# Performance work log

Measured on AMD Instinct MI355X. Metric: run time of the kernel, lower is better.

The kernel has to match this reference:

```python
import jax, jax.numpy as jnp
import numpy as np

B, L, D, H = 4, 2048, 512, 512


def setup_inputs() -> dict:
    key = jax.random.key(0)
    ks = jax.random.split(key, 7)
    scale = D ** (-0.5)
    return {
        "x": jax.random.normal(ks[0], (B, L, D), jnp.float32),
        "hidden": jax.random.normal(ks[1], (B, D, H), jnp.float32),
        "log_base_lr": jnp.asarray(np.log(0.01), jnp.float32),
        "log_base_weight_decay": jnp.asarray(np.log(0.99), jnp.float32),
        "Wq": jax.random.normal(ks[2], (H, D), jnp.float32) * scale,
        "Wk": jax.random.normal(ks[3], (H, D), jnp.float32) * scale,
        "Wv": jax.random.normal(ks[4], (D, D), jnp.float32) * scale,
        "fc_lr_w": jax.random.normal(ks[5], (1, D), jnp.float32) * scale,
        "fc_lr_b": jnp.zeros((1,), jnp.float32),
        "fc_wd_w": jax.random.normal(ks[6], (1, D), jnp.float32) * scale,
        "fc_wd_b": jnp.zeros((1,), jnp.float32),
    }


def reference(x, hidden, log_base_lr, log_base_weight_decay, Wq, Wk, Wv,
              fc_lr_w, fc_lr_b, fc_wd_w, fc_wd_b):
    b, l, d = x.shape
    W_prev = hidden                                      # (b, d, h)
    query = jnp.einsum('bld,hd->blh', x, Wq)             # (b, l, h)
    key = jnp.einsum('bld,hd->blh', x, Wk)               # (b, l, h)
    value = jnp.einsum('bld,ed->ble', x, Wv)             # (b, l, d)

    lr = jnp.exp(log_base_lr) * jax.nn.sigmoid(
        jnp.einsum('bld,d->bl', x, fc_lr_w[0]) + fc_lr_b[0])        # (b, l)
    log_weight_decay = jnp.log(
        jnp.exp(log_base_weight_decay) * jax.nn.sigmoid(
            jnp.einsum('bld,d->bl', x, fc_wd_w[0]) + fc_wd_b[0]))   # (b, l)

    # cross-chunk decay: exp of prefix-sum of log decays
    wd_cross = jnp.exp(jnp.cumsum(log_weight_decay, axis=1))        # (b, l)

    # inner-chunk decay mask: (b, m, l), strictly-upper cumsum then upper triu
    rep = jnp.broadcast_to(log_weight_decay[:, None, :], (b, l, l))
    wd_inner = jnp.triu(jnp.exp(jnp.cumsum(jnp.triu(rep, 1), axis=2)))

    kq = jnp.einsum('blh,bmh->blm', key, query)          # (b, l, m)
    mask_kq = kq * wd_inner                              # (b, l, m)

    WpK_V = jnp.einsum('bdh,blh->bld', W_prev, key) - value         # (b, l, d)

    y_inner = -jnp.einsum('bld,bl,blm->bld', WpK_V, lr, mask_kq)
    y_cross = jnp.einsum('bdh,blh,bl->bld', W_prev, key, wd_cross)
    y = y_inner + y_cross

    W_next_inner = -jnp.einsum('bld,bl,blh->bdh', WpK_V, lr * wd_inner[:, :, -1], key)
    W_next_cross = W_prev * wd_cross[:, -1][:, None, None]
    W_next = W_next_inner + W_next_cross
    return (y, W_next)
```

## Files before the change

### kernel.cpp

```cpp
#include <hip/hip_runtime.h>
#include <cstdint>
#include <cstddef>

#define B_ 4
#define L_ 2048
#define D_ 512
#define H_ 512
#define CH 64
#define NC (L_ / CH)
#define NS 4

typedef unsigned short u16;
typedef __attribute__((ext_vector_type(8))) short short8v;
typedef __attribute__((ext_vector_type(4))) float f32x4;

typedef __attribute__((address_space(3))) unsigned lds_uint;
typedef const __attribute__((address_space(1))) unsigned glob_uint;

__device__ __forceinline__ void glds16(const u16* g, const u16* l) {
    __builtin_amdgcn_global_load_lds((glob_uint*)g, (lds_uint*)l, 16, 0, 0);
}

__device__ __forceinline__ u16 bf16_rne(float x) {
    union { float f; unsigned u; } v; v.f = x;
    unsigned r = v.u + 0x7fffu + ((v.u >> 16) & 1u);
    return (u16)(r >> 16);
}
__device__ __forceinline__ float bf16_tof(u16 h) {
    union { unsigned u; float f; } v; v.u = ((unsigned)h) << 16;
    return v.f;
}

__global__ __launch_bounds__(256) void k_prep(
    const float* __restrict__ x, const float* __restrict__ flr_w, const float* __restrict__ flr_b,
    const float* __restrict__ fwd_w, const float* __restrict__ fwd_b,
    const float* __restrict__ lblr, const float* __restrict__ lbwd,
    float* __restrict__ lr, float* __restrict__ lwd, float* __restrict__ wd,
    u16* __restrict__ xh)
{
    int bx = blockIdx.x;
    int wave = threadIdx.x >> 6;
    int lane = threadIdx.x & 63;
    int row  = bx * 4 + wave;
    const float4* xr = (const float4*)(x + (size_t)row * D_);
    const float4* wl = (const float4*)flr_w;
    const float4* ww = (const float4*)fwd_w;
    float zl = 0.f, zw = 0.f;
#pragma unroll
    for (int i = 0; i < 2; ++i) {
        int idx = lane + i * 64;
        float4 xv = xr[idx];
        float4 av = wl[idx];
        float4 bv = ww[idx];
        zl += xv.x*av.x + xv.y*av.y + xv.z*av.z + xv.w*av.w;
        zw += xv.x*bv.x + xv.y*bv.y + xv.z*bv.z + xv.w*bv.w;
        ushort4 h4;
        h4.x = bf16_rne(xv.x); h4.y = bf16_rne(xv.y);
        h4.z = bf16_rne(xv.z); h4.w = bf16_rne(xv.w);
        *(ushort4*)(xh + (size_t)row * D_ + idx * 4) = h4;
    }
#pragma unroll
    for (int off = 32; off; off >>= 1) {
        zl += __shfl_xor(zl, off, 64);
        zw += __shfl_xor(zw, off, 64);
    }
    if (lane == 0) {
        zl += flr_b[0];
        zw += fwd_b[0];
        float lrv = expf(lblr[0]) / (1.f + expf(-zl));
        float ls = (zw >= 0.f) ? (-log1pf(expf(-zw))) : (zw - log1pf(expf(zw)));
        float lw = lbwd[0] + ls;
        lr[row]  = lrv;
        lwd[row] = lw;
        wd[row]  = expf(lw);
    }
}

__global__ __launch_bounds__(256) void k_cumsum(
    const float* __restrict__ lwd, const float* __restrict__ lr,
    const float* __restrict__ Wq, const float* __restrict__ Wk, const float* __restrict__ Wv,
    const float* __restrict__ hid,
    u16* __restrict__ Wqh, u16* __restrict__ Wkh, u16* __restrict__ Wvh, u16* __restrict__ Wph,
    float* __restrict__ cum, float* __restrict__ wdc, float* __restrict__ c)
{
    int bx = blockIdx.x;
    if (bx >= B_) {
        int idx = bx - B_;
        int y = idx >> 8;
        const size_t DH = (size_t)D_ * H_;
        const float* s; u16* d;
        if      (y == 0) { s = Wq; d = Wqh; }
        else if (y == 1) { s = Wk; d = Wkh; }
        else if (y == 2) { s = Wv; d = Wvh; }
        else             { s = hid + (size_t)(y - 3) * DH; d = Wph + (size_t)(y - 3) * DH; }
        int i = ((idx & 255) * 256 + threadIdx.x) * 4;
        float4 v = *(const float4*)(s + i);
        ushort4 h4;
        h4.x = bf16_rne(v.x); h4.y = bf16_rne(v.y);
        h4.z = bf16_rne(v.z); h4.w = bf16_rne(v.w);
        *(ushort4*)(d + i) = h4;
        return;
    }
    int b = bx;
    int t = threadIdx.x;
    const float* in = lwd + (size_t)b * L_;
    float v[8];
    float s = 0.f;
#pragma unroll
    for (int j = 0; j < 8; ++j) { s += in[t*8 + j]; v[j] = s; }
    __shared__ float sd[256];
    __shared__ float totb;
    sd[t] = s;
    __syncthreads();
    for (int d = 1; d < 256; d <<= 1) {
        float xv = (t >= d) ? sd[t - d] : 0.f;
        __syncthreads();
        sd[t] += xv;
        __syncthreads();
    }
    float excl = sd[t] - s;
    if (t == 255) totb = sd[255];
    __syncthreads();
    float total = totb;
#pragma unroll
    for (int j = 0; j < 8; ++j) {
        int l = t*8 + j;
        float cv = excl + v[j];
        cum[(size_t)b*L_ + l] = cv;
        wdc[(size_t)b*L_ + l] = expf(cv);
        c[(size_t)b*L_ + l]   = lr[(size_t)b*L_ + l] * expf(total - cv);
    }
}


__device__ __forceinline__ void gg64(int lda, int ldb, int m0, int n0,
                                     size_t& gA, size_t& gB, int& dst,
                                     int offA[2][4], int offB[2][2]) {
    const int tid = threadIdx.x;
    const int lane = tid & 63;
    const int wv = tid >> 6, wm = wv >> 2, wn = wv & 3;
    int r = tid >> 3, s = tid & 7;
    int sg = s ^ ((r >> 1) & 7);
    gA = (size_t)(m0 + r) * lda + sg * 8;
    gB = (size_t)(n0 + r) * ldb + sg * 8;
    dst = wv * 1024;
#pragma unroll
    for (int ks = 0; ks < 2; ++ks) {
#pragma unroll
        for (int f = 0; f < 4; ++f) {
            int ra = wm * 64 + f * 16 + (lane & 15);
            offA[ks][f] = ra * 128 + (((ks * 4 + (lane >> 4)) ^ ((ra >> 1) & 7)) * 16);
        }
#pragma unroll
        for (int f = 0; f < 2; ++f) {
            int rb = wn * 32 + f * 16 + (lane & 15);
            offB[ks][f] = rb * 128 + (((ks * 4 + (lane >> 4)) ^ ((rb >> 1) & 7)) * 16);
        }
    }
}

__device__ __forceinline__ void core8_dualB(
    char* smem, const u16* __restrict__ A_g,
    const u16* __restrict__ B0_g, const u16* __restrict__ B1_g,
    int lda, int ldb, int K, int m0, int n0, f32x4 acc0[4][2], f32x4 acc1[4][2])
{
    size_t gA, gB; int dst; int offA[2][4], offB[2][2];
    gg64(lda, ldb, m0, n0, gA, gB, dst, offA, offB);
    const size_t hA = (size_t)64 * lda, hB = (size_t)64 * ldb;
    auto stage = [&](int bi, int k0) {
        glds16(A_g  + gA + k0,      (const u16*)(smem + bi * 16384 + dst));
        glds16(A_g  + gA + hA + k0, (const u16*)(smem + bi * 16384 + 8192 + dst));
        glds16(B0_g + gB + k0,      (const u16*)(smem + 49152 + bi * 16384 + dst));
        glds16(B0_g + gB + hB + k0, (const u16*)(smem + 49152 + bi * 16384 + 8192 + dst));
        glds16(B1_g + gB + k0,      (const u16*)(smem + 98304 + bi * 16384 + dst));
        glds16(B1_g + gB + hB + k0, (const u16*)(smem + 98304 + bi * 16384 + 8192 + dst));
    };
    const int nt = K >> 6;
    stage(0, 0);
    if (nt > 1) stage(1, 64);
    int bi = 0, bs = 2;
    for (int t = 0; t < nt; ++t) {
        if (t + 1 < nt) asm volatile("s_waitcnt vmcnt(6)" ::: "memory");
        else            asm volatile("s_waitcnt vmcnt(0)" ::: "memory");
        __builtin_amdgcn_s_barrier();
        asm volatile("" ::: "memory");
        if (t + 2 < nt) stage(bs, (t + 2) << 6);
        const char* bA  = smem + bi * 16384;
        const char* bB0 = smem + 49152 + bi * 16384;
        const char* bB1 = smem + 98304 + bi * 16384;
#pragma unroll
        for (int ks = 0; ks < 2; ++ks) {
            short8v a0 = *(const short8v*)(bA + offA[ks][0]);
            short8v a1 = *(const short8v*)(bA + offA[ks][1]);
            short8v a2 = *(const short8v*)(bA + offA[ks][2]);
            short8v a3 = *(const short8v*)(bA + offA[ks][3]);
            short8v p0 = *(const short8v*)(bB0 + offB[ks][0]);
            short8v p1 = *(const short8v*)(bB0 + offB[ks][1]);
            short8v q0 = *(const short8v*)(bB1 + offB[ks][0]);
            short8v q1 = *(const short8v*)(bB1 + offB[ks][1]);
            __builtin_amdgcn_s_setprio(1);
            acc0[0][0] = __builtin_amdgcn_mfma_f32_16x16x32_bf16(a0, p0, acc0[0][0], 0, 0, 0);
            acc0[0][1] = __builtin_amdgcn_mfma_f32_16x16x32_bf16(a0, p1, acc0[0][1], 0, 0, 0);
            acc0[1][0] = __builtin_amdgcn_mfma_f32_16x16x32_bf16(a1, p0, acc0[1][0], 0, 0, 0);
            acc0[1][1] = __builtin_amdgcn_mfma_f32_16x16x32_bf16(a1, p1, acc0[1][1], 0, 0, 0);
            acc0[2][0] = __builtin_amdgcn_mfma_f32_16x16x32_bf16(a2, p0, acc0[2][0], 0, 0, 0);
            acc0[2][1] = __builtin_amdgcn_mfma_f32_16x16x32_bf16(a2, p1, acc0[2][1], 0, 0, 0);
            acc0[3][0] = __builtin_amdgcn_mfma_f32_16x16x32_bf16(a3, p0, acc0[3][0], 0, 0, 0);
            acc0[3][1] = __builtin_amdgcn_mfma_f32_16x16x32_bf16(a3, p1, acc0[3][1], 0, 0, 0);
            acc1[0][0] = __builtin_amdgcn_mfma_f32_16x16x32_bf16(a0, q0, acc1[0][0], 0, 0, 0);
            acc1[0][1] = __builtin_amdgcn_mfma_f32_16x16x32_bf16(a0, q1, acc1[0][1], 0, 0, 0);
            acc1[1][0] = __builtin_amdgcn_mfma_f32_16x16x32_bf16(a1, q0, acc1[1][0], 0, 0, 0);
            acc1[1][1] = __builtin_amdgcn_mfma_f32_16x16x32_bf16(a1, q1, acc1[1][1], 0, 0, 0);
            acc1[2][0] = __builtin_amdgcn_mfma_f32_16x16x32_bf16(a2, q0, acc1[2][0], 0, 0, 0);
            acc1[2][1] = __builtin_amdgcn_mfma_f32_16x16x32_bf16(a2, q1, acc1[2][1], 0, 0, 0);
            acc1[3][0] = __builtin_amdgcn_mfma_f32_16x16x32_bf16(a3, q0, acc1[3][0], 0, 0, 0);
            acc1[3][1] = __builtin_amdgcn_mfma_f32_16x16x32_bf16(a3, q1, acc1[3][1], 0, 0, 0);
            __builtin_amdgcn_s_setprio(0);
        }
        asm volatile("" ::: "memory");
        bi = (bi == 2) ? 0 : bi + 1;
        bs = (bs == 2) ? 0 : bs + 1;
    }
    asm volatile("" ::: "memory");
    __builtin_amdgcn_s_barrier();
}

__device__ __forceinline__ void core8_dualAB(
    char* smem, const u16* __restrict__ A0_g, const u16* __restrict__ A1_g,
    const u16* __restrict__ B0_g, const u16* __restrict__ B1_g,
    int lda, int ldb, int K, int m0, int n0, f32x4 acc0[4][2], f32x4 acc1[4][2])
{
    size_t gA, gB; int dst; int offA[2][4], offB[2][2];
    gg64(lda, ldb, m0, n0, gA, gB, dst, offA, offB);
    const size_t hA = (size_t)64 * lda, hB = (size_t)64 * ldb;
    auto stage = [&](int bi, int k0) {
        glds16(A0_g + gA + k0,      (const u16*)(smem + bi * 16384 + dst));
        glds16(A0_g + gA + hA + k0, (const u16*)(smem + bi * 16384 + 8192 + dst));
        glds16(A1_g + gA + k0,      (const u16*)(smem + 32768 + bi * 16384 + dst));
        glds16(A1_g + gA + hA + k0, (const u16*)(smem + 32768 + bi * 16384 + 8192 + dst));
        glds16(B0_g + gB + k0,      (const u16*)(smem + 65536 + bi * 16384 + dst));
        glds16(B0_g + gB + hB + k0, (const u16*)(smem + 65536 + bi * 16384 + 8192 + dst));
        glds16(B1_g + gB + k0,      (const u16*)(smem + 98304 + bi * 16384 + dst));
        glds16(B1_g + gB + hB + k0, (const u16*)(smem + 98304 + bi * 16384 + 8192 + dst));
    };
    const int nt = K >> 6;
    stage(0, 0);
    if (nt > 1) stage(1, 64);
    for (int t = 0; t < nt; ++t) {
        const int bi = t & 1;
        if (t + 1 < nt) asm volatile("s_waitcnt vmcnt(8)" ::: "memory");
        else            asm volatile("s_waitcnt vmcnt(0)" ::: "memory");
        __builtin_amdgcn_s_barrier();
        asm volatile("" ::: "memory");
        const char* bA0 = smem + bi * 16384;
        const char* bA1 = smem + 32768 + bi * 16384;
        const char* bB0 = smem + 65536 + bi * 16384;
        const char* bB1 = smem + 98304 + bi * 16384;
#pragma unroll
        for (int ks = 0; ks < 2; ++ks) {
            short8v a0 = *(const short8v*)(bA0 + offA[ks][0]);
            short8v a1 = *(const short8v*)(bA0 + offA[ks][1]);
            short8v a2 = *(const short8v*)(bA0 + offA[ks][2]);
            short8v a3 = *(const short8v*)(bA0 + offA[ks][3]);
            short8v c0 = *(const short8v*)(bA1 + offA[ks][0]);
            short8v c1 = *(const short8v*)(bA1 + offA[ks][1]);
            short8v c2 = *(const short8v*)(bA1 + offA[ks][2]);
            short8v c3 = *(const short8v*)(bA1 + offA[ks][3]);
            short8v p0 = *(const short8v*)(bB0 + offB[ks][0]);
            short8v p1 = *(const short8v*)(bB0 + offB[ks][1]);
            short8v q0 = *(const short8v*)(bB1 + offB[ks][0]);
            short8v q1 = *(const short8v*)(bB1 + offB[ks][1]);
            __builtin_amdgcn_s_setprio(1);
            acc0[0][0] = __builtin_amdgcn_mfma_f32_16x16x32_bf16(a0, p0, acc0[0][0], 0, 0, 0);
            acc0[0][1] = __builtin_amdgcn_mfma_f32_16x16x32_bf16(a0, p1, acc0[0][1], 0, 0, 0);
            acc0[1][0] = __builtin_amdgcn_mfma_f32_16x16x32_bf16(a1, p0, acc0[1][0], 0, 0, 0);
            acc0[1][1] = __builtin_amdgcn_mfma_f32_16x16x32_bf16(a1, p1, acc0[1][1], 0, 0, 0);
            acc0[2][0] = __builtin_amdgcn_mfma_f32_16x16x32_bf16(a2, p0, acc0[2][0], 0, 0, 0);
            acc0[2][1] = __builtin_amdgcn_mfma_f32_16x16x32_bf16(a2, p1, acc0[2][1], 0, 0, 0);
            acc0[3][0] = __builtin_amdgcn_mfma_f32_16x16x32_bf16(a3, p0, acc0[3][0], 0, 0, 0);
            acc0[3][1] = __builtin_amdgcn_mfma_f32_16x16x32_bf16(a3, p1, acc0[3][1], 0, 0, 0);
            acc1[0][0] = __builtin_amdgcn_mfma_f32_16x16x32_bf16(c0, q0, acc1[0][0], 0, 0, 0);
            acc1[0][1] = __builtin_amdgcn_mfma_f32_16x16x32_bf16(c0, q1, acc1[0][1], 0, 0, 0);
            acc1[1][0] = __builtin_amdgcn_mfma_f32_16x16x32_bf16(c1, q0, acc1[1][0], 0, 0, 0);
            acc1[1][1] = __builtin_amdgcn_mfma_f32_16x16x32_bf16(c1, q1, acc1[1][1], 0, 0, 0);
            acc1[2][0] = __builtin_amdgcn_mfma_f32_16x16x32_bf16(c2, q0, acc1[2][0], 0, 0, 0);
            acc1[2][1] = __builtin_amdgcn_mfma_f32_16x16x32_bf16(c2, q1, acc1[2][1], 0, 0, 0);
            acc1[3][0] = __builtin_amdgcn_mfma_f32_16x16x32_bf16(c3, q0, acc1[3][0], 0, 0, 0);
            acc1[3][1] = __builtin_amdgcn_mfma_f32_16x16x32_bf16(c3, q1, acc1[3][1], 0, 0, 0);
            __builtin_amdgcn_s_setprio(0);
        }
        asm volatile("" ::: "memory");
        __builtin_amdgcn_s_barrier();
        asm volatile("" ::: "memory");
        if (t + 2 < nt) stage(bi, (t + 2) << 6);
    }
}

__device__ __forceinline__ void core8_single(
    char* smem, const u16* __restrict__ A_g, const u16* __restrict__ B_g,
    int lda, int ldb, int K, int m0, int n0, f32x4 acc[4][2])
{
    size_t gA, gB; int dst; int offA[2][4], offB[2][2];
    gg64(lda, ldb, m0, n0, gA, gB, dst, offA, offB);
    const size_t hA = (size_t)64 * lda, hB = (size_t)64 * ldb;
    auto stage = [&](int bi, int k0) {
        glds16(A_g + gA + k0,      (const u16*)(smem + bi * 16384 + dst));
        glds16(A_g + gA + hA + k0, (const u16*)(smem + bi * 16384 + 8192 + dst));
        glds16(B_g + gB + k0,      (const u16*)(smem + 49152 + bi * 16384 + dst));
        glds16(B_g + gB + hB + k0, (const u16*)(smem + 49152 + bi * 16384 + 8192 + dst));
    };
    const int nt = K >> 6;
    stage(0, 0);
    if (nt > 1) stage(1, 64);
    int bi = 0, bs = 2;
    for (int t = 0; t < nt; ++t) {
        if (t + 1 < nt) asm volatile("s_waitcnt vmcnt(4)" ::: "memory");
        else            asm volatile("s_waitcnt vmcnt(0)" ::: "memory");
        __builtin_amdgcn_s_barrier();
        asm volatile("" ::: "memory");
        if (t + 2 < nt) stage(bs, (t + 2) << 6);
        const char* bA = smem + bi * 16384;
        const char* bB = smem + 49152 + bi * 16384;
#pragma unroll
        for (int ks = 0; ks < 2; ++ks) {
            short8v a0 = *(const short8v*)(bA + offA[ks][0]);
            short8v a1 = *(const short8v*)(bA + offA[ks][1]);
            short8v a2 = *(const short8v*)(bA + offA[ks][2]);
            short8v a3 = *(const short8v*)(bA + offA[ks][3]);
            short8v p0 = *(const short8v*)(bB + offB[ks][0]);
            short8v p1 = *(const short8v*)(bB + offB[ks][1]);
            __builtin_amdgcn_s_setprio(1);
            acc[0][0] = __builtin_amdgcn_mfma_f32_16x16x32_bf16(a0, p0, acc[0][0], 0, 0, 0);
            acc[0][1] = __builtin_amdgcn_mfma_f32_16x16x32_bf16(a0, p1, acc[0][1], 0, 0, 0);
            acc[1][0] = __builtin_amdgcn_mfma_f32_16x16x32_bf16(a1, p0, acc[1][0], 0, 0, 0);
            acc[1][1] = __builtin_amdgcn_mfma_f32_16x16x32_bf16(a1, p1, acc[1][1], 0, 0, 0);
            acc[2][0] = __builtin_amdgcn_mfma_f32_16x16x32_bf16(a2, p0, acc[2][0], 0, 0, 0);
            acc[2][1] = __builtin_amdgcn_mfma_f32_16x16x32_bf16(a2, p1, acc[2][1], 0, 0, 0);
            acc[3][0] = __builtin_amdgcn_mfma_f32_16x16x32_bf16(a3, p0, acc[3][0], 0, 0, 0);
            acc[3][1] = __builtin_amdgcn_mfma_f32_16x16x32_bf16(a3, p1, acc[3][1], 0, 0, 0);
            __builtin_amdgcn_s_setprio(0);
        }
        asm volatile("" ::: "memory");
        bi = (bi == 2) ? 0 : bi + 1;
        bs = (bs == 2) ? 0 : bs + 1;
    }
    asm volatile("" ::: "memory");
    __builtin_amdgcn_s_barrier();
}

__global__ __launch_bounds__(512) void k_mfma_qk(
    const u16* __restrict__ xh,
    const u16* __restrict__ Wqh, const u16* __restrict__ Wkh,
    const float* __restrict__ cvec, const float* __restrict__ wd,
    u16* __restrict__ kh, u16* __restrict__ kcth, u16* __restrict__ Gloc)
{
    __shared__ __align__(16) char smem[147456];
    __shared__ float pwd[128];
    int flat = blockIdx.x;
    flat = (flat & 7) * 32 + (flat >> 3);
    int n0 = (flat & 3) * 128;
    int m0 = (flat >> 2) * 128;
    f32x4 accq[4][2], acck[4][2];
#pragma unroll
    for (int i = 0; i < 4; ++i)
#pragma unroll
    for (int j = 0; j < 2; ++j) { accq[i][j] = 0.f; acck[i][j] = 0.f; }
    core8_dualB(smem, xh, Wqh, Wkh, D_, D_, D_, m0, n0, accq, acck);

    const int lane = threadIdx.x & 63;
    const int wv = threadIdx.x >> 6, wm = wv >> 2, wn = wv & 3;
    const int colq = lane & 15, rq = lane >> 4;

#pragma unroll
    for (int mf = 0; mf < 4; ++mf) {
        int grow0 = m0 + wm*64 + mf*16 + rq*4;
        float cv[4];
#pragma unroll
        for (int r = 0; r < 4; ++r) cv[r] = cvec[grow0 + r];
#pragma unroll
        for (int nf = 0; nf < 2; ++nf) {
            int gc = n0 + wn*32 + nf*16 + colq;
            f32x4 a = acck[mf][nf];
            ushort4 hc;
#pragma unroll
            for (int r = 0; r < 4; ++r) {
                kh[(size_t)(grow0 + r) * H_ + gc] = bf16_rne(a[r]);
                ((u16*)&hc)[r] = bf16_rne(cv[r] * a[r]);
            }
            int b = grow0 >> 11, lloc = grow0 & 2047;
            size_t tbase = (size_t)b * (H_ * L_) + (size_t)gc * L_ + lloc;
            *(ushort4*)(kcth + tbase) = hc;
        }
    }

    u16* g = (u16*)smem;
#pragma unroll
    for (int mf = 0; mf < 4; ++mf) {
        int rl0 = wm*64 + mf*16 + rq*4;
#pragma unroll
        for (int nf = 0; nf < 2; ++nf) {
            int cl = wn*32 + nf*16 + colq;
#pragma unroll
            for (int r = 0; r < 4; ++r)
                g[(rl0 + r)*128 + cl] = bf16_rne(accq[mf][nf][r]);
        }
    }
    if (threadIdx.x < 128) pwd[threadIdx.x] = wd[m0 + threadIdx.x];
    __syncthreads();
    if (threadIdx.x < 256) {
        int col  = threadIdx.x & 127;
        int base = (threadIdx.x >> 7) * 64;
        float G = bf16_tof(g[(base + 63)*128 + col]);
        for (int l = 62; l >= 0; --l) {
            float qv = bf16_tof(g[(base + l)*128 + col]);
            G = fmaf(pwd[base + l + 1], G, qv);
            g[(base + l)*128 + col] = bf16_rne(G);
        }
    }
    __syncthreads();
    int row = threadIdx.x >> 2, c0 = (threadIdx.x & 3) * 32;
    u16* dst = Gloc + (size_t)(m0 + row) * H_ + n0 + c0;
#pragma unroll
    for (int j = 0; j < 4; ++j)
        *(int4*)(dst + j*8) = *(const int4*)&g[row*128 + c0 + j*8];
}

__global__ __launch_bounds__(64) void k_scan_carry(
    const float* __restrict__ cum, const u16* __restrict__ Gloc, float* __restrict__ Gs)
{
    int b = blockIdx.x;
    int h = blockIdx.y * 64 + threadIdx.x;
    __shared__ float dec[NC];
    const float* cb = cum + (size_t)b * L_;
    if (threadIdx.x < NC - 1) dec[threadIdx.x] = expf(cb[(threadIdx.x + 1) * CH] - cb[threadIdx.x * CH]);
    __syncthreads();
    const u16* g = Gloc + (size_t)b * L_ * H_ + h;
    float* gs = Gs + (size_t)b * NC * H_ + h;
    float v[NC];
#pragma unroll
    for (int c = 0; c < NC; ++c)
        v[c] = bf16_tof(g[(size_t)(c * CH) * H_]);
    float G = v[NC - 1];
    gs[(size_t)(NC - 1) * H_] = G;
#pragma unroll
    for (int c = NC - 2; c >= 0; --c) {
        G = fmaf(dec[c], G, v[c]);
        gs[(size_t)c * H_] = G;
    }
}

__global__ __launch_bounds__(256) void k_sdot(
    const u16* __restrict__ kh,
    const u16* __restrict__ Gloc, const float* __restrict__ Gs,
    const float* __restrict__ cum, float* __restrict__ S)
{
    int wave = threadIdx.x >> 6, lane = threadIdx.x & 63;
    int row = blockIdx.x * 4 + wave;
    int b = row >> 11, l = row & 2047;
    int c = l / CH;
    float a = 0.f;
    const float* gsr = Gs;
    if (c < NC - 1) {
        a = expf(cum[((size_t)b << 11) + (size_t)((c + 1) * CH)] - cum[row]);
        gsr = Gs + ((size_t)(b * NC + c + 1)) * H_;
    }
    const u16* khr = kh + (size_t)row * H_;
    const u16* glr = Gloc + (size_t)row * H_;
    const float4* gq = (const float4*)gsr;
    float s = 0.f;
    int base = lane * 8;
    ushort4 h0 = *(const ushort4*)(khr + base);
    ushort4 h1 = *(const ushort4*)(khr + base + 4);
    ushort4 g0 = *(const ushort4*)(glr + base);
    ushort4 g1 = *(const ushort4*)(glr + base + 4);
    float4 s0 = gq[lane * 2];
    float4 s1 = gq[lane * 2 + 1];
    s += bf16_tof(h0.x) * fmaf(a, s0.x, bf16_tof(g0.x));
    s += bf16_tof(h0.y) * fmaf(a, s0.y, bf16_tof(g0.y));
    s += bf16_tof(h0.z) * fmaf(a, s0.z, bf16_tof(g0.z));
    s += bf16_tof(h0.w) * fmaf(a, s0.w, bf16_tof(g0.w));
    s += bf16_tof(h1.x) * fmaf(a, s1.x, bf16_tof(g1.x));
    s += bf16_tof(h1.y) * fmaf(a, s1.y, bf16_tof(g1.y));
    s += bf16_tof(h1.z) * fmaf(a, s1.z, bf16_tof(g1.z));
    s += bf16_tof(h1.w) * fmaf(a, s1.w, bf16_tof(g1.w));
#pragma unroll
    for (int off = 32; off; off >>= 1) s += __shfl_xor(s, off, 64);
    if (lane == 0) S[row] = s;
}

__global__ __launch_bounds__(512) void k_mfma_ev(
    const u16* __restrict__ kh, const u16* __restrict__ xh,
    const u16* __restrict__ Wph, const u16* __restrict__ Wvh,
    const float* __restrict__ lr, const float* __restrict__ S, const float* __restrict__ wdc,
    float* __restrict__ y, u16* __restrict__ Eth)
{
    __shared__ __align__(16) char smem[131072];
    int flat = blockIdx.x;
    flat = (flat & 7) * 32 + (flat >> 3);
    int n0 = (flat & 3) * 128;
    int m0 = ((flat >> 2) & 15) * 128;
    int b  = flat >> 6;
    f32x4 acce[4][2], accv[4][2];
#pragma unroll
    for (int i = 0; i < 4; ++i)
#pragma unroll
    for (int j = 0; j < 2; ++j) { acce[i][j] = 0.f; accv[i][j] = 0.f; }
    core8_dualAB(smem, kh + (size_t)b * L_ * H_, xh + (size_t)b * L_ * D_,
                 Wph + (size_t)b * D_ * H_, Wvh,
                 H_, H_, H_, m0, n0, acce, accv);

    const int lane = threadIdx.x & 63;
    const int wv = threadIdx.x >> 6, wm = wv >> 2, wn = wv & 3;
    const int colq = lane & 15, rq = lane >> 4;
#pragma unroll
    for (int mf = 0; mf < 4; ++mf) {
        int grow0 = m0 + wm*64 + mf*16 + rq*4;
        float ayv[4], wdv[4];
#pragma unroll
        for (int r = 0; r < 4; ++r) {
            size_t grow = (size_t)b * L_ + grow0 + r;
            ayv[r] = -lr[grow] * S[grow];
            wdv[r] = wdc[grow];
        }
#pragma unroll
        for (int nf = 0; nf < 2; ++nf) {
            int gc = n0 + wn*32 + nf*16 + colq;
            f32x4 ae = acce[mf][nf];
            f32x4 av = accv[mf][nf];
            ushort4 he;
#pragma unroll
            for (int r = 0; r < 4; ++r) {
                size_t gi = ((size_t)b * L_ + grow0 + r) * D_ + gc;
                float e = ae[r] - av[r];
                y[gi] = e * ayv[r] + ae[r] * wdv[r];
                ((u16*)&he)[r] = bf16_rne(e);
            }
            size_t tbase = (size_t)b * (D_ * L_) + (size_t)gc * L_ + grow0;
            *(ushort4*)(Eth + tbase) = he;
        }
    }
}

__global__ __launch_bounds__(512) void k_mfma_wn(
    const u16* __restrict__ Eth, const u16* __restrict__ kcth,
    u16* __restrict__ wp)
{
    __shared__ __align__(16) char smem[98304];
    int flat = blockIdx.x;
    flat = (flat & 7) * 32 + (flat >> 3);
    int n0 = (flat & 3) * 128;
    int m0 = ((flat >> 2) & 3) * 128;
    int z  = flat >> 4;
    int b = z >> 2, s = z & 3;
    f32x4 acc[4][2];
#pragma unroll
    for (int i = 0; i < 4; ++i)
#pragma unroll
    for (int j = 0; j < 2; ++j) acc[i][j] = 0.f;
    const size_t pa = (size_t)b * (D_ * L_) + (size_t)s * (L_ / NS);
    const size_t pb = (size_t)b * (H_ * L_) + (size_t)s * (L_ / NS);
    core8_single(smem, Eth + pa, kcth + pb, L_, L_, L_ / NS, m0, n0, acc);

    u16* out = wp + (size_t)z * D_ * H_;
    const int lane = threadIdx.x & 63;
    const int wv = threadIdx.x >> 6, wm = wv >> 2, wn = wv & 3;
    const int colq = lane & 15, rq = lane >> 4;
#pragma unroll
    for (int mf = 0; mf < 4; ++mf) {
        int grow0 = m0 + wm*64 + mf*16 + rq*4;
#pragma unroll
        for (int nf = 0; nf < 2; ++nf) {
            int gc = n0 + wn*32 + nf*16 + colq;
            f32x4 a = acc[mf][nf];
#pragma unroll
            for (int r = 0; r < 4; ++r) out[(size_t)(grow0 + r) * H_ + gc] = bf16_rne(a[r]);
        }
    }
}

__global__ __launch_bounds__(256) void k_wnext_reduce(
    const float* __restrict__ Wp, const u16* __restrict__ wp, const float* __restrict__ wdc,
    float* __restrict__ outw)
{
    size_t g = (size_t)blockIdx.x * 256 + threadIdx.x;
    size_t per = (size_t)D_ * H_ / 4;
    int b = (int)(g / per);
    size_t r = g % per;
    float wl = wdc[(size_t)b * L_ + (L_ - 1)];
    float4 w0 = ((const float4*)Wp)[g];
    float4 o;
    o.x = wl * w0.x; o.y = wl * w0.y; o.z = wl * w0.z; o.w = wl * w0.w;
#pragma unroll
    for (int s = 0; s < NS; ++s) {
        ushort4 p = ((const ushort4*)wp)[(size_t)(b * NS + s) * per + r];
        o.x -= bf16_tof(p.x); o.y -= bf16_tof(p.y);
        o.z -= bf16_tof(p.z); o.w -= bf16_tof(p.w);
    }
    ((float4*)outw)[g] = o;
}

extern "C" void kernel_launch(void* const* d_in, const int* in_sizes, int n_in,
                              void* d_out, int out_size, void* d_ws, size_t ws_size,
                              hipStream_t stream)
{
    (void)in_sizes; (void)n_in; (void)out_size; (void)ws_size;
    const float* x    = (const float*)d_in[0];
    const float* hid  = (const float*)d_in[1];
    const float* lblr = (const float*)d_in[2];
    const float* lbwd = (const float*)d_in[3];
    const float* Wq   = (const float*)d_in[4];
    const float* Wk   = (const float*)d_in[5];
    const float* Wv   = (const float*)d_in[6];
    const float* flrw = (const float*)d_in[7];
    const float* flrb = (const float*)d_in[8];
    const float* fwdw = (const float*)d_in[9];
    const float* fwdb = (const float*)d_in[10];
    float* out = (float*)d_out;

    const size_t BL  = (size_t)B_ * L_;
    const size_t BLH = BL * H_;
    const size_t DH  = (size_t)D_ * H_;

    char* w = (char*)d_ws;
    u16* Gloc_  = (u16*)w;   w += BLH * 2;
    u16* xh_    = (u16*)w;   w += BLH * 2;
    u16* kh_    = (u16*)w;   w += BLH * 2;
    u16* kcth_  = (u16*)w;   w += BLH * 2;
    u16* Eth_   = (u16*)w;   w += BLH * 2;
    u16* Wqh_   = (u16*)w;   w += DH * 2;
    u16* Wkh_   = (u16*)w;   w += DH * 2;
    u16* Wvh_   = (u16*)w;   w += DH * 2;
    u16* Wph_   = (u16*)w;   w += (size_t)B_ * DH * 2;
    float* lr_  = (float*)w; w += BL * 4;
    float* lwd_ = (float*)w; w += BL * 4;
    float* wd_  = (float*)w; w += BL * 4;
    float* cum_ = (float*)w; w += BL * 4;
    float* wdc_ = (float*)w; w += BL * 4;
    float* c_   = (float*)w; w += BL * 4;
    float* S_   = (float*)w; w += BL * 4;
    float* Gs_  = (float*)w; w += (size_t)B_ * NC * H_ * 4;

    u16* wp_ = Gloc_;

    k_prep<<<2048, 256, 0, stream>>>(x, flrw, flrb, fwdw, fwdb, lblr, lbwd,
                                     lr_, lwd_, wd_, xh_);
    k_cumsum<<<B_ + 7 * 256, 256, 0, stream>>>(lwd_, lr_, Wq, Wk, Wv, hid,
                                               Wqh_, Wkh_, Wvh_, Wph_,
                                               cum_, wdc_, c_);
    k_mfma_qk<<<256, 512, 0, stream>>>(xh_, Wqh_, Wkh_, c_, wd_,
                                       kh_, kcth_, Gloc_);
    k_scan_carry<<<dim3(B_, 8), 64, 0, stream>>>(cum_, Gloc_, Gs_);
    k_sdot<<<2048, 256, 0, stream>>>(kh_, Gloc_, Gs_, cum_, S_);
    k_mfma_ev<<<256, 512, 0, stream>>>(kh_, xh_, Wph_, Wvh_,
                                       lr_, S_, wdc_, out, Eth_);
    k_mfma_wn<<<256, 512, 0, stream>>>(Eth_, kcth_, wp_);
    k_wnext_reduce<<<1024, 256, 0, stream>>>(hid, wp_, wdc_, out + BLH);
}
```

Measured before the change: 69.64 us.

## Load shared Wv B-operand directly from global and use triple-buffered LDS pipeline

In the dual-GEMM core for the E/V kernel, the Wv operand (shared across batches, likely L2-resident) is no longer staged through LDS. Each lane reads its MFMA fragment straight from global memory at the start of each K tile. The remaining three operands move to a three-stage LDS ring, which removes the trailing barrier per iteration and issues the next stage earlier. LDS use grows to 144KB, and the kernel now depends on fast cached global reads for Wv, whose latency sits directly before the MFMAs.

Result: slower. 73.57 us (+5.6%).

```diff
diff --git a/kernel.cpp b/kernel.cpp
--- a/kernel.cpp
+++ b/kernel.cpp
@@ -225,37 +225,49 @@
     __builtin_amdgcn_s_barrier();
 }
 
-__device__ __forceinline__ void core8_dualAB(
+__device__ __forceinline__ void core8_dualAB_bl2(
     char* smem, const u16* __restrict__ A0_g, const u16* __restrict__ A1_g,
     const u16* __restrict__ B0_g, const u16* __restrict__ B1_g,
     int lda, int ldb, int K, int m0, int n0, f32x4 acc0[4][2], f32x4 acc1[4][2])
 {
     size_t gA, gB; int dst; int offA[2][4], offB[2][2];
     gg64(lda, ldb, m0, n0, gA, gB, dst, offA, offB);
+    const int lane = threadIdx.x & 63;
+    const int wn = (threadIdx.x >> 6) & 3;
+    const u16* b1p[2][2];
+#pragma unroll
+    for (int ks = 0; ks < 2; ++ks)
+#pragma unroll
+        for (int f = 0; f < 2; ++f)
+            b1p[ks][f] = B1_g + (size_t)(n0 + wn*32 + f*16 + (lane & 15)) * ldb
+                              + (ks * 4 + (lane >> 4)) * 8;
     const size_t hA = (size_t)64 * lda, hB = (size_t)64 * ldb;
     auto stage = [&](int bi, int k0) {
         glds16(A0_g + gA + k0,      (const u16*)(smem + bi * 16384 + dst));
         glds16(A0_g + gA + hA + k0, (const u16*)(smem + bi * 16384 + 8192 + dst));
-        glds16(A1_g + gA + k0,      (const u16*)(smem + 32768 + bi * 16384 + dst));
-        glds16(A1_g + gA + hA + k0, (const u16*)(smem + 32768 + bi * 16384 + 8192 + dst));
-        glds16(B0_g + gB + k0,      (const u16*)(smem + 65536 + bi * 16384 + dst));
-        glds16(B0_g + gB + hB + k0, (const u16*)(smem + 65536 + bi * 16384 + 8192 + dst));
-        glds16(B1_g + gB + k0,      (const u16*)(smem + 98304 + bi * 16384 + dst));
-        glds16(B1_g + gB + hB + k0, (const u16*)(smem + 98304 + bi * 16384 + 8192 + dst));
+        glds16(A1_g + gA + k0,      (const u16*)(smem + 49152 + bi * 16384 + dst));
+        glds16(A1_g + gA + hA + k0, (const u16*)(smem + 49152 + bi * 16384 + 8192 + dst));
+        glds16(B0_g + gB + k0,      (const u16*)(smem + 98304 + bi * 16384 + dst));
+        glds16(B0_g + gB + hB + k0, (const u16*)(smem + 98304 + bi * 16384 + 8192 + dst));
     };
     const int nt = K >> 6;
     stage(0, 0);
     if (nt > 1) stage(1, 64);
+    int bi = 0, bs = 2;
     for (int t = 0; t < nt; ++t) {
-        const int bi = t & 1;
-        if (t + 1 < nt) asm volatile("s_waitcnt vmcnt(8)" ::: "memory");
+        if (t + 1 < nt) asm volatile("s_waitcnt vmcnt(6)" ::: "memory");
         else            asm volatile("s_waitcnt vmcnt(0)" ::: "memory");
         __builtin_amdgcn_s_barrier();
         asm volatile("" ::: "memory");
+        const int kcur = t << 6;
+        short8v q00 = *(const short8v*)(b1p[0][0] + kcur);
+        short8v q01 = *(const short8v*)(b1p[0][1] + kcur);
+        short8v q10 = *(const short8v*)(b1p[1][0] + kcur);
+        short8v q11 = *(const short8v*)(b1p[1][1] + kcur);
+        if (t + 2 < nt) stage(bs, (t + 2) << 6);
         const char* bA0 = smem + bi * 16384;
-        const char* bA1 = smem + 32768 + bi * 16384;
-        const char* bB0 = smem + 65536 + bi * 16384;
-        const char* bB1 = smem + 98304 + bi * 16384;
+        const char* bA1 = smem + 49152 + bi * 16384;
+        const char* bB0 = smem + 98304 + bi * 16384;
 #pragma unroll
         for (int ks = 0; ks < 2; ++ks) {
             short8v a0 = *(const short8v*)(bA0 + offA[ks][0]);
@@ -268,8 +280,8 @@
             short8v c3 = *(const short8v*)(bA1 + offA[ks][3]);
             short8v p0 = *(const short8v*)(bB0 + offB[ks][0]);
             short8v p1 = *(const short8v*)(bB0 + offB[ks][1]);
-            short8v q0 = *(const short8v*)(bB1 + offB[ks][0]);
-            short8v q1 = *(const short8v*)(bB1 + offB[ks][1]);
+            short8v q0 = ks ? q10 : q00;
+            short8v q1 = ks ? q11 : q01;
             __builtin_amdgcn_s_setprio(1);
             acc0[0][0] = __builtin_amdgcn_mfma_f32_16x16x32_bf16(a0, p0, acc0[0][0], 0, 0, 0);
             acc0[0][1] = __builtin_amdgcn_mfma_f32_16x16x32_bf16(a0, p1, acc0[0][1], 0, 0, 0);
@@ -290,9 +302,8 @@
             __builtin_amdgcn_s_setprio(0);
         }
         asm volatile("" ::: "memory");
-        __builtin_amdgcn_s_barrier();
-        asm volatile("" ::: "memory");
-        if (t + 2 < nt) stage(bi, (t + 2) << 6);
+        bi = (bi == 2) ? 0 : bi + 1;
+        bs = (bs == 2) ? 0 : bs + 1;
     }
 }
 
@@ -494,7 +505,7 @@
     const float* __restrict__ lr, const float* __restrict__ S, const float* __restrict__ wdc,
     float* __restrict__ y, u16* __restrict__ Eth)
 {
-    __shared__ __align__(16) char smem[131072];
+    __shared__ __align__(16) char smem[147456];
     int flat = blockIdx.x;
     flat = (flat & 7) * 32 + (flat >> 3);
     int n0 = (flat & 3) * 128;
@@ -505,9 +516,9 @@
     for (int i = 0; i < 4; ++i)
 #pragma unroll
     for (int j = 0; j < 2; ++j) { acce[i][j] = 0.f; accv[i][j] = 0.f; }
-    core8_dualAB(smem, kh + (size_t)b * L_ * H_, xh + (size_t)b * L_ * D_,
-                 Wph + (size_t)b * D_ * H_, Wvh,
-                 H_, H_, H_, m0, n0, acce, accv);
+    core8_dualAB_bl2(smem, kh + (size_t)b * L_ * H_, xh + (size_t)b * L_ * D_,
+                     Wph + (size_t)b * D_ * H_, Wvh,
+                     H_, H_, H_, m0, n0, acce, accv);
 
     const int lane = threadIdx.x & 63;
     const int wv = threadIdx.x >> 6, wm = wv >> 2, wn = wv & 3;
```
